# Performance work log

Hardware: AMD Instinct MI355X
Metric: run time of the kernel (lower is better)

Reference implementation:

```python
import jax, jax.numpy as jnp
import numpy as np

N, E, H, L, G, MAX_Z = 100000, 1600000, 128, 3, 1024, 1000
BN_EPS = 1e-5

def setup_inputs() -> dict:
    key = jax.random.key(0)
    ks = jax.random.split(key, 16)
    z = jax.random.randint(ks[0], (N,), 0, MAX_Z)
    edge_index = jax.random.randint(ks[1], (2, E), 0, N)
    batch = jnp.sort(jax.random.randint(ks[2], (N,), 0, G))
    s = 1.0 / np.sqrt(H)
    z_table = jax.random.normal(ks[3], (MAX_Z, H), jnp.float32)
    conv_W1 = jax.random.normal(ks[4], (L, H, H), jnp.float32) * s
    conv_b1 = jnp.zeros((L, H), jnp.float32)
    conv_W2 = jax.random.normal(ks[5], (L, H, H), jnp.float32) * s
    conv_b2 = jnp.zeros((L, H), jnp.float32)
    bn_gamma = jnp.ones((L, H), jnp.float32)
    bn_beta = jnp.zeros((L, H), jnp.float32)
    lin1_W = jax.random.normal(ks[6], (L * H, H), jnp.float32) / np.sqrt(L * H)
    lin1_b = jnp.zeros((H,), jnp.float32)
    lin2_W = jax.random.normal(ks[7], (H, 1), jnp.float32) * s
    lin2_b = jnp.zeros((1,), jnp.float32)
    return {"z": z, "edge_index": edge_index, "batch": batch,
            "z_table": z_table, "conv_W1": conv_W1, "conv_b1": conv_b1,
            "conv_W2": conv_W2, "conv_b2": conv_b2, "bn_gamma": bn_gamma,
            "bn_beta": bn_beta, "lin1_W": lin1_W, "lin1_b": lin1_b,
            "lin2_W": lin2_W, "lin2_b": lin2_b}

def _gin_layer(x, src, dst, W1, b1, W2, b2, gamma, beta):
    # GIN sum aggregation: (1+eps)*x_i + sum_{j->i} x_j  (eps=0)
    agg = x + jax.ops.segment_sum(x[src], dst, num_segments=N)
    h = jax.nn.relu(agg @ W1 + b1)
    h = jax.nn.relu(h @ W2 + b2)
    # BatchNorm1d (training-mode batch statistics over nodes)
    mu = jnp.mean(h, axis=0)
    var = jnp.mean(jnp.square(h - mu), axis=0)
    return gamma * (h - mu) * jax.lax.rsqrt(var + BN_EPS) + beta

def reference(z, edge_index, batch, z_table, conv_W1, conv_b1, conv_W2,
              conv_b2, bn_gamma, bn_beta, lin1_W, lin1_b, lin2_W, lin2_b):
    src, dst = edge_index[0], edge_index[1]
    x = z_table[z]                      # [N, H]
    xs = []
    for l in range(L):
        x = _gin_layer(x, src, dst, conv_W1[l], conv_b1[l], conv_W2[l],
                       conv_b2[l], bn_gamma[l], bn_beta[l])
        xs.append(x)
    feat = jnp.concatenate(xs, axis=1)  # [N, L*H] (jk=True)
    sums = jax.ops.segment_sum(feat, batch, num_segments=G)
    cnt = jax.ops.segment_sum(jnp.ones((N,), feat.dtype), batch, num_segments=G)
    pooled = sums / jnp.maximum(cnt, 1.0)[:, None]   # global_mean_pool [G, L*H]
    h = jax.nn.relu(pooled @ lin1_W + lin1_b)
    # dropout inactive (eval mode)
    return h @ lin2_W + lin2_b          # [G, 1]
```

## Files before the change

kernel.cpp:

```cpp
#include <hip/hip_runtime.h>

#define NN 100000
#define NE 1600000
#define HD 128
#define NL 3
#define NG 1024
#define BN_EPS 1e-5f
#define SCAN_CHUNK 1024

static inline int cdiv(int a, int b) { return (a + b - 1) / b; }

__global__ __launch_bounds__(256) void zero_counts_kernel(int* __restrict__ cnt) {
  int t = blockIdx.x * 256 + threadIdx.x;
  if (t < NN) cnt[t] = 0;
}

__global__ __launch_bounds__(256) void hist_kernel(const int* __restrict__ dstI,
    int* __restrict__ cnt) {
  int e = blockIdx.x * 256 + threadIdx.x;
  if (e < NE) atomicAdd(&cnt[dstI[e]], 1);
}

__global__ __launch_bounds__(256) void scan_block_kernel(const int* __restrict__ cnt,
    int* __restrict__ rowptr, int* __restrict__ bsums) {
  __shared__ int sh[SCAN_CHUNK];
  __shared__ int ts[256];
  int base = blockIdx.x * SCAN_CHUNK;
  for (int i = threadIdx.x; i < SCAN_CHUNK; i += 256)
    sh[i] = (base + i < NN) ? cnt[base + i] : 0;
  __syncthreads();
  int t4 = threadIdx.x * 4;
  int a0 = sh[t4], a1 = sh[t4 + 1], a2 = sh[t4 + 2], a3 = sh[t4 + 3];
  int tsum = a0 + a1 + a2 + a3;
  ts[threadIdx.x] = tsum;
  __syncthreads();
  for (int off = 1; off < 256; off <<= 1) {
    int v = ts[threadIdx.x];
    int u = (threadIdx.x >= off) ? ts[threadIdx.x - off] : 0;
    __syncthreads();
    ts[threadIdx.x] = v + u;
    __syncthreads();
  }
  int texcl = ts[threadIdx.x] - tsum;
  sh[t4] = texcl;
  sh[t4 + 1] = texcl + a0;
  sh[t4 + 2] = texcl + a0 + a1;
  sh[t4 + 3] = texcl + a0 + a1 + a2;
  __syncthreads();
  for (int i = threadIdx.x; i < SCAN_CHUNK; i += 256) {
    int g = base + i;
    if (g < NN) rowptr[g] = sh[i];
  }
  if (threadIdx.x == 255) bsums[blockIdx.x] = ts[255];
}

__global__ void scan_bsums_kernel(int* __restrict__ bsums, int nb) {
  if (threadIdx.x == 0) {
    int run = 0;
    for (int i = 0; i < nb; ++i) { int v = bsums[i]; bsums[i] = run; run += v; }
  }
}

__global__ __launch_bounds__(256) void scan_add_kernel(int* __restrict__ rowptr,
    const int* __restrict__ bsums, int* __restrict__ fill_off) {
  int t = blockIdx.x * 256 + threadIdx.x;
  if (t < NN) {
    int v = rowptr[t] + bsums[t / SCAN_CHUNK];
    rowptr[t] = v;
    fill_off[t] = v;
  }
  if (t == 0) rowptr[NN] = NE;
}

__global__ __launch_bounds__(256) void fill_kernel(const int* __restrict__ srcI,
    const int* __restrict__ dstI, const int* __restrict__ z,
    int* __restrict__ fill_off, int* __restrict__ esrc, int* __restrict__ esrcz) {
  int e = blockIdx.x * 256 + threadIdx.x;
  if (e >= NE) return;
  int s = srcI[e];
  int d = dstI[e];
  int pos = atomicAdd(&fill_off[d], 1);
  esrc[pos] = s;
  esrcz[pos] = z[s];
}

__global__ __launch_bounds__(256) void agg_kernel(const int* __restrict__ rowptr,
    const int* __restrict__ eidx, const float* __restrict__ xsrc, int xstride,
    const int* __restrict__ selfz, float* __restrict__ agg) {
  int n = blockIdx.x * 4 + (threadIdx.x >> 6);
  if (n >= NN) return;
  int lane = threadIdx.x & 63;
  int lo = rowptr[n], hi = rowptr[n + 1];
  int deg = hi - lo;
  int selfrow = selfz ? selfz[n] : n;
  float2 acc = *(const float2*)(xsrc + (size_t)selfrow * xstride + lane * 2);

  for (int base = 0; base < deg; base += 64) {
    int cnt = deg - base; if (cnt > 64) cnt = 64;
    int idx = (base + lane < deg) ? eidx[lo + base + lane] : 0;
    int j = 0;
    for (; j + 4 <= cnt; j += 4) {
      int s0 = __shfl(idx, j, 64);
      int s1 = __shfl(idx, j + 1, 64);
      int s2 = __shfl(idx, j + 2, 64);
      int s3 = __shfl(idx, j + 3, 64);
      float2 v0 = *(const float2*)(xsrc + (size_t)s0 * xstride + lane * 2);
      float2 v1 = *(const float2*)(xsrc + (size_t)s1 * xstride + lane * 2);
      float2 v2 = *(const float2*)(xsrc + (size_t)s2 * xstride + lane * 2);
      float2 v3 = *(const float2*)(xsrc + (size_t)s3 * xstride + lane * 2);
      acc.x += v0.x + v1.x + v2.x + v3.x;
      acc.y += v0.y + v1.y + v2.y + v3.y;
    }
    for (; j < cnt; ++j) {
      int s = __shfl(idx, j, 64);
      float2 v = *(const float2*)(xsrc + (size_t)s * xstride + lane * 2);
      acc.x += v.x; acc.y += v.y;
    }
  }
  *(float2*)(agg + (size_t)n * HD + lane * 2) = acc;
}

template <int STATS>
__global__ __launch_bounds__(256) void gemm_relu_kernel_t(
    const float* __restrict__ A, const float* __restrict__ B,
    const float* __restrict__ bias, float* __restrict__ C, int M,
    double* __restrict__ gsums) {
  __shared__ float As[128][65];
  __shared__ float Bs[32][128];
  __shared__ float csum[256];
  const int tid = threadIdx.x;
  const int row0 = blockIdx.x * 64;

  if (STATS) { csum[tid] = 0.f; }

  #pragma unroll
  for (int i = 0; i < 8; ++i) {
    int f = tid + i * 256;
    int row = f >> 5;
    int kq = (f & 31) << 2;
    int gr = row0 + row;
    float4 v = make_float4(0.f, 0.f, 0.f, 0.f);
    if (gr < M) v = *(const float4*)(A + (size_t)gr * HD + kq);
    As[kq + 0][row] = v.x; As[kq + 1][row] = v.y;
    As[kq + 2][row] = v.z; As[kq + 3][row] = v.w;
  }

  const int colbase = (tid & 15) << 2;
  const int rowbase = (tid >> 4) << 2;
  float acc[4][8] = {};

  for (int kc = 0; kc < 4; ++kc) {
    __syncthreads();
    #pragma unroll
    for (int i = 0; i < 4; ++i) {
      int f = tid + i * 256;
      int k = f >> 5;
      int c4 = (f & 31) << 2;
      *(float4*)(&Bs[k][c4]) = *(const float4*)(B + (size_t)(kc * 32 + k) * HD + c4);
    }
    __syncthreads();
    #pragma unroll
    for (int k = 0; k < 32; ++k) {
      const int kk = kc * 32 + k;
      float a0 = As[kk][rowbase + 0];
      float a1 = As[kk][rowbase + 1];
      float a2 = As[kk][rowbase + 2];
      float a3 = As[kk][rowbase + 3];
      float4 bl = *(const float4*)(&Bs[k][colbase]);
      float4 bh = *(const float4*)(&Bs[k][colbase + 64]);
      acc[0][0] += a0 * bl.x; acc[0][1] += a0 * bl.y; acc[0][2] += a0 * bl.z; acc[0][3] += a0 * bl.w;
      acc[0][4] += a0 * bh.x; acc[0][5] += a0 * bh.y; acc[0][6] += a0 * bh.z; acc[0][7] += a0 * bh.w;
      acc[1][0] += a1 * bl.x; acc[1][1] += a1 * bl.y; acc[1][2] += a1 * bl.z; acc[1][3] += a1 * bl.w;
      acc[1][4] += a1 * bh.x; acc[1][5] += a1 * bh.y; acc[1][6] += a1 * bh.z; acc[1][7] += a1 * bh.w;
      acc[2][0] += a2 * bl.x; acc[2][1] += a2 * bl.y; acc[2][2] += a2 * bl.z; acc[2][3] += a2 * bl.w;
      acc[2][4] += a2 * bh.x; acc[2][5] += a2 * bh.y; acc[2][6] += a2 * bh.z; acc[2][7] += a2 * bh.w;
      acc[3][0] += a3 * bl.x; acc[3][1] += a3 * bl.y; acc[3][2] += a3 * bl.z; acc[3][3] += a3 * bl.w;
      acc[3][4] += a3 * bh.x; acc[3][5] += a3 * bh.y; acc[3][6] += a3 * bh.z; acc[3][7] += a3 * bh.w;
    }
  }

  float4 bvl = *(const float4*)(bias + colbase);
  float4 bvh = *(const float4*)(bias + colbase + 64);
  float ps[8] = {}, pq[8] = {};
  #pragma unroll
  for (int r = 0; r < 4; ++r) {
    int gr = row0 + rowbase + r;
    if (gr < M) {
      float4 o;
      o.x = fmaxf(acc[r][0] + bvl.x, 0.f);
      o.y = fmaxf(acc[r][1] + bvl.y, 0.f);
      o.z = fmaxf(acc[r][2] + bvl.z, 0.f);
      o.w = fmaxf(acc[r][3] + bvl.w, 0.f);
      *(float4*)(C + (size_t)gr * HD + colbase) = o;
      if (STATS) {
        ps[0] += o.x; ps[1] += o.y; ps[2] += o.z; ps[3] += o.w;
        pq[0] += o.x * o.x; pq[1] += o.y * o.y; pq[2] += o.z * o.z; pq[3] += o.w * o.w;
      }
      o.x = fmaxf(acc[r][4] + bvh.x, 0.f);
      o.y = fmaxf(acc[r][5] + bvh.y, 0.f);
      o.z = fmaxf(acc[r][6] + bvh.z, 0.f);
      o.w = fmaxf(acc[r][7] + bvh.w, 0.f);
      *(float4*)(C + (size_t)gr * HD + colbase + 64) = o;
      if (STATS) {
        ps[4] += o.x; ps[5] += o.y; ps[6] += o.z; ps[7] += o.w;
        pq[4] += o.x * o.x; pq[5] += o.y * o.y; pq[6] += o.z * o.z; pq[7] += o.w * o.w;
      }
    }
  }

  if (STATS) {
    __syncthreads();
    #pragma unroll
    for (int c = 0; c < 4; ++c) {
      atomicAdd(&csum[colbase + c], ps[c]);
      atomicAdd(&csum[128 + colbase + c], pq[c]);
      atomicAdd(&csum[colbase + 64 + c], ps[4 + c]);
      atomicAdd(&csum[128 + colbase + 64 + c], pq[4 + c]);
    }
    __syncthreads();
    if (tid < 128) {
      atomicAdd(&gsums[tid], (double)csum[tid]);
      atomicAdd(&gsums[HD + tid], (double)csum[128 + tid]);
    }
  }
}

__global__ void zero_d_kernel(double* p) { p[threadIdx.x] = 0.0; }

__global__ void bn_finalize_kernel(const double* __restrict__ sums,
    const float* __restrict__ gamma, const float* __restrict__ beta,
    float* __restrict__ ss) {
  int c = threadIdx.x;
  double mu = sums[c] * (1.0 / NN);
  double var = sums[HD + c] * (1.0 / NN) - mu * mu;
  float sc = gamma[c] * (float)(1.0 / sqrt(var + (double)BN_EPS));
  ss[c] = sc;
  ss[HD + c] = beta[c] - (float)mu * sc;
}

__global__ __launch_bounds__(256) void bn_apply_kernel(const float* __restrict__ h,
    const float* __restrict__ ss, float* __restrict__ featl) {
  int t = blockIdx.x * 256 + threadIdx.x;
  if (t >= NN * 32) return;
  int row = t >> 5, c4 = (t & 31) << 2;
  float4 v = *(const float4*)(h + (size_t)row * HD + c4);
  float4 sc = *(const float4*)(ss + c4);
  float4 sh = *(const float4*)(ss + HD + c4);
  float4 o;
  o.x = v.x * sc.x + sh.x;
  o.y = v.y * sc.y + sh.y;
  o.z = v.z * sc.z + sh.z;
  o.w = v.w * sc.w + sh.w;
  *(float4*)(featl + (size_t)row * (NL * HD) + c4) = o;
}

__device__ __forceinline__ int lbound(const int* __restrict__ b, int val) {
  int lo = 0, hi = NN;
  while (lo < hi) { int m = (lo + hi) >> 1; if (b[m] < val) lo = m + 1; else hi = m; }
  return lo;
}

__global__ __launch_bounds__(384) void pool_kernel(const int* __restrict__ batch,
    const float* __restrict__ feat, float* __restrict__ pooled) {
  int g = blockIdx.x;
  int lo = lbound(batch, g), hi = lbound(batch, g + 1);
  float s = 0.f;
  for (int r = lo; r < hi; ++r) s += feat[(size_t)r * (NL * HD) + threadIdx.x];
  float inv = 1.f / (float)max(hi - lo, 1);
  pooled[(size_t)g * (NL * HD) + threadIdx.x] = s * inv;
}

__global__ __launch_bounds__(128) void mlp_kernel(const float* __restrict__ pooled,
    const float* __restrict__ W1, const float* __restrict__ b1,
    const float* __restrict__ W2, const float* __restrict__ b2,
    float* __restrict__ out) {
  int g = blockIdx.x, c = threadIdx.x;
  const float* p = pooled + (size_t)g * (NL * HD);
  float acc = b1[c];
  #pragma unroll 4
  for (int k = 0; k < NL * HD; ++k) acc = fmaf(p[k], W1[(size_t)k * HD + c], acc);
  acc = fmaxf(acc, 0.f);
  float prod = acc * W2[c];
  #pragma unroll
  for (int off = 32; off > 0; off >>= 1) prod += __shfl_xor(prod, off, 64);
  __shared__ float part[2];
  if ((c & 63) == 0) part[c >> 6] = prod;
  __syncthreads();
  if (c == 0) out[g] = part[0] + part[1] + b2[0];
}

extern "C" void kernel_launch(void* const* d_in, const int* in_sizes, int n_in,
                              void* d_out, int out_size, void* d_ws, size_t ws_size,
                              hipStream_t stream) {
  (void)in_sizes; (void)n_in; (void)out_size; (void)ws_size;
  const int*   z     = (const int*)d_in[0];
  const int*   ei    = (const int*)d_in[1];
  const int*   batch = (const int*)d_in[2];
  const float* ztab  = (const float*)d_in[3];
  const float* W1    = (const float*)d_in[4];
  const float* b1    = (const float*)d_in[5];
  const float* W2    = (const float*)d_in[6];
  const float* b2    = (const float*)d_in[7];
  const float* gamma = (const float*)d_in[8];
  const float* beta  = (const float*)d_in[9];
  const float* l1W   = (const float*)d_in[10];
  const float* l1b   = (const float*)d_in[11];
  const float* l2W   = (const float*)d_in[12];
  const float* l2b   = (const float*)d_in[13];
  float* out = (float*)d_out;

  char* w = (char*)d_ws;
  float*  bufA   = (float*)w;  w += (size_t)NN * HD * 4;
  float*  bufB   = (float*)w;  w += (size_t)NN * HD * 4;
  float*  feat   = (float*)w;  w += (size_t)NN * (NL * HD) * 4;
  float*  pooled = (float*)w;  w += (size_t)NG * (NL * HD) * 4;
  double* sums   = (double*)w; w += 256 * 8;
  float*  sshift = (float*)w;  w += 256 * 4;
  int*    rowptr = (int*)w;    w += (size_t)(NN + 1) * 4;
  int*    counts = (int*)w;    w += (size_t)NN * 4;
  int*    filloff= (int*)w;    w += (size_t)NN * 4;
  int*    esrc   = (int*)w;    w += (size_t)NE * 4;
  int*    bsums  = (int*)w;    w += (size_t)cdiv(NN, SCAN_CHUNK) * 4;
  int* esrcz = (int*)bufA;

  const int* srcI = ei;
  const int* dstI = ei + NE;

  dim3 blk(256);
  const int g_nh = cdiv(NN * 32, 256);
  const int g_nn = cdiv(NN, 256);
  const int g_ne = cdiv(NE, 256);
  const int nb_scan = cdiv(NN, SCAN_CHUNK);

  zero_counts_kernel<<<g_nn, blk, 0, stream>>>(counts);
  hist_kernel<<<g_ne, blk, 0, stream>>>(dstI, counts);
  scan_block_kernel<<<nb_scan, blk, 0, stream>>>(counts, rowptr, bsums);
  scan_bsums_kernel<<<1, 64, 0, stream>>>(bsums, nb_scan);
  scan_add_kernel<<<g_nn, blk, 0, stream>>>(rowptr, bsums, filloff);
  fill_kernel<<<g_ne, blk, 0, stream>>>(srcI, dstI, z, filloff, esrc, esrcz);

  for (int l = 0; l < NL; ++l) {
    float* aggbuf = (l & 1) ? bufA : bufB;
    float* tmpbuf = (l & 1) ? bufB : bufA;

    if (l == 0) {
      agg_kernel<<<cdiv(NN, 4), blk, 0, stream>>>(rowptr, esrcz, ztab, HD, z, aggbuf);
    } else {
      agg_kernel<<<cdiv(NN, 4), blk, 0, stream>>>(rowptr, esrc,
          feat + (l - 1) * HD, NL * HD, nullptr, aggbuf);
    }
    gemm_relu_kernel_t<0><<<cdiv(NN, 64), blk, 0, stream>>>(aggbuf,
        W1 + (size_t)l * HD * HD, b1 + l * HD, tmpbuf, NN, nullptr);
    zero_d_kernel<<<1, 256, 0, stream>>>(sums);
    gemm_relu_kernel_t<1><<<cdiv(NN, 64), blk, 0, stream>>>(tmpbuf,
        W2 + (size_t)l * HD * HD, b2 + l * HD, aggbuf, NN, sums);
    bn_finalize_kernel<<<1, 128, 0, stream>>>(sums, gamma + l * HD, beta + l * HD, sshift);
    bn_apply_kernel<<<g_nh, blk, 0, stream>>>(aggbuf, sshift, feat + l * HD);
  }

  pool_kernel<<<NG, 384, 0, stream>>>(batch, feat, pooled);
  mlp_kernel<<<NG, 128, 0, stream>>>(pooled, l1W, l1b, l2W, l2b, out);
}
```

Before: 1.200 ms.

## Fold BatchNorm affine into aggregation and pooling; use 128x128 GEMM tiles

Drops the standalone BN-apply pass. The second GEMM now writes the raw ReLU output straight into the concatenated feature buffer. The per-channel scale and shift are applied later, at aggregation time as scale*sum + (deg+1)*shift, and in the pooling kernel, which is exact because the affine is linear. The GEMM is also retiled to 128 rows per block, with an 8x8 register tile per thread and A loaded per k-chunk, to raise arithmetic intensity. This removes one full read and write of the hidden activations per layer, at the cost of more registers per thread and possibly lower occupancy.

```diff
diff --git a/kernel.cpp b/kernel.cpp
--- a/kernel.cpp
+++ b/kernel.cpp
@@ -86,7 +86,8 @@
 
 __global__ __launch_bounds__(256) void agg_kernel(const int* __restrict__ rowptr,
     const int* __restrict__ eidx, const float* __restrict__ xsrc, int xstride,
-    const int* __restrict__ selfz, float* __restrict__ agg) {
+    const int* __restrict__ selfz, const float* __restrict__ ss,
+    float* __restrict__ agg) {
   int n = blockIdx.x * 4 + (threadIdx.x >> 6);
   if (n >= NN) return;
   int lane = threadIdx.x & 63;
@@ -117,105 +118,96 @@
       acc.x += v.x; acc.y += v.y;
     }
   }
-  *(float2*)(agg + (size_t)n * HD + lane * 2) = acc;
+
+  float2 o = acc;
+  if (ss) {
+    float scx = ss[lane * 2], scy = ss[lane * 2 + 1];
+    float shx = ss[128 + lane * 2], shy = ss[129 + lane * 2];
+    float cntf = (float)(deg + 1);
+    o.x = acc.x * scx + cntf * shx;
+    o.y = acc.y * scy + cntf * shy;
+  }
+  *(float2*)(agg + (size_t)n * HD + lane * 2) = o;
 }
 
 template <int STATS>
-__global__ __launch_bounds__(256) void gemm_relu_kernel_t(
+__global__ __launch_bounds__(256) void gemm128_kernel(
     const float* __restrict__ A, const float* __restrict__ B,
-    const float* __restrict__ bias, float* __restrict__ C, int M,
+    const float* __restrict__ bias, float* __restrict__ C, int cstride, int M,
     double* __restrict__ gsums) {
-  __shared__ float As[128][65];
-  __shared__ float Bs[32][128];
+  __shared__ float As[32][136];
+  __shared__ float Bs[32][136];
   __shared__ float csum[256];
   const int tid = threadIdx.x;
-  const int row0 = blockIdx.x * 64;
-
-  if (STATS) { csum[tid] = 0.f; }
-
-  #pragma unroll
-  for (int i = 0; i < 8; ++i) {
-    int f = tid + i * 256;
-    int row = f >> 5;
-    int kq = (f & 31) << 2;
-    int gr = row0 + row;
-    float4 v = make_float4(0.f, 0.f, 0.f, 0.f);
-    if (gr < M) v = *(const float4*)(A + (size_t)gr * HD + kq);
-    As[kq + 0][row] = v.x; As[kq + 1][row] = v.y;
-    As[kq + 2][row] = v.z; As[kq + 3][row] = v.w;
-  }
-
-  const int colbase = (tid & 15) << 2;
-  const int rowbase = (tid >> 4) << 2;
-  float acc[4][8] = {};
+  const int row0 = blockIdx.x * 128;
+  const int tr = tid >> 4;
+  const int tc = tid & 15;
+
+  if (STATS) csum[tid] = 0.f;
+
+  float acc[8][8] = {};
 
   for (int kc = 0; kc < 4; ++kc) {
     __syncthreads();
     #pragma unroll
     for (int i = 0; i < 4; ++i) {
       int f = tid + i * 256;
-      int k = f >> 5;
-      int c4 = (f & 31) << 2;
+      int row = f >> 3, kq = f & 7;
+      int gr = row0 + row;
+      float4 v = make_float4(0.f, 0.f, 0.f, 0.f);
+      if (gr < M) v = *(const float4*)(A + (size_t)gr * HD + kc * 32 + kq * 4);
+      As[kq * 4 + 0][row] = v.x; As[kq * 4 + 1][row] = v.y;
+      As[kq * 4 + 2][row] = v.z; As[kq * 4 + 3][row] = v.w;
+    }
+    #pragma unroll
+    for (int i = 0; i < 4; ++i) {
+      int f = tid + i * 256;
+      int k = f >> 5, c4 = (f & 31) << 2;
       *(float4*)(&Bs[k][c4]) = *(const float4*)(B + (size_t)(kc * 32 + k) * HD + c4);
     }
     __syncthreads();
     #pragma unroll
     for (int k = 0; k < 32; ++k) {
-      const int kk = kc * 32 + k;
-      float a0 = As[kk][rowbase + 0];
-      float a1 = As[kk][rowbase + 1];
-      float a2 = As[kk][rowbase + 2];
-      float a3 = As[kk][rowbase + 3];
-      float4 bl = *(const float4*)(&Bs[k][colbase]);
-      float4 bh = *(const float4*)(&Bs[k][colbase + 64]);
-      acc[0][0] += a0 * bl.x; acc[0][1] += a0 * bl.y; acc[0][2] += a0 * bl.z; acc[0][3] += a0 * bl.w;
-      acc[0][4] += a0 * bh.x; acc[0][5] += a0 * bh.y; acc[0][6] += a0 * bh.z; acc[0][7] += a0 * bh.w;
-      acc[1][0] += a1 * bl.x; acc[1][1] += a1 * bl.y; acc[1][2] += a1 * bl.z; acc[1][3] += a1 * bl.w;
-      acc[1][4] += a1 * bh.x; acc[1][5] += a1 * bh.y; acc[1][6] += a1 * bh.z; acc[1][7] += a1 * bh.w;
-      acc[2][0] += a2 * bl.x; acc[2][1] += a2 * bl.y; acc[2][2] += a2 * bl.z; acc[2][3] += a2 * bl.w;
-      acc[2][4] += a2 * bh.x; acc[2][5] += a2 * bh.y; acc[2][6] += a2 * bh.z; acc[2][7] += a2 * bh.w;
-      acc[3][0] += a3 * bl.x; acc[3][1] += a3 * bl.y; acc[3][2] += a3 * bl.z; acc[3][3] += a3 * bl.w;
-      acc[3][4] += a3 * bh.x; acc[3][5] += a3 * bh.y; acc[3][6] += a3 * bh.z; acc[3][7] += a3 * bh.w;
-    }
-  }
-
-  float4 bvl = *(const float4*)(bias + colbase);
-  float4 bvh = *(const float4*)(bias + colbase + 64);
+      float4 a0 = *(const float4*)(&As[k][tr * 8]);
+      float4 a1 = *(const float4*)(&As[k][tr * 8 + 4]);
+      float4 b0 = *(const float4*)(&Bs[k][tc * 8]);
+      float4 b1 = *(const float4*)(&Bs[k][tc * 8 + 4]);
+      float av[8] = {a0.x, a0.y, a0.z, a0.w, a1.x, a1.y, a1.z, a1.w};
+      float bv[8] = {b0.x, b0.y, b0.z, b0.w, b1.x, b1.y, b1.z, b1.w};
+      #pragma unroll
+      for (int r = 0; r < 8; ++r)
+        #pragma unroll
+        for (int c = 0; c < 8; ++c)
+          acc[r][c] += av[r] * bv[c];
+    }
+  }
+
+  float4 bv0 = *(const float4*)(bias + tc * 8);
+  float4 bv1 = *(const float4*)(bias + tc * 8 + 4);
+  float bb[8] = {bv0.x, bv0.y, bv0.z, bv0.w, bv1.x, bv1.y, bv1.z, bv1.w};
   float ps[8] = {}, pq[8] = {};
   #pragma unroll
-  for (int r = 0; r < 4; ++r) {
-    int gr = row0 + rowbase + r;
+  for (int r = 0; r < 8; ++r) {
+    int gr = row0 + tr * 8 + r;
     if (gr < M) {
-      float4 o;
-      o.x = fmaxf(acc[r][0] + bvl.x, 0.f);
-      o.y = fmaxf(acc[r][1] + bvl.y, 0.f);
-      o.z = fmaxf(acc[r][2] + bvl.z, 0.f);
-      o.w = fmaxf(acc[r][3] + bvl.w, 0.f);
-      *(float4*)(C + (size_t)gr * HD + colbase) = o;
+      float o[8];
+      #pragma unroll
+      for (int c = 0; c < 8; ++c) o[c] = fmaxf(acc[r][c] + bb[c], 0.f);
+      *(float4*)(C + (size_t)gr * cstride + tc * 8)     = make_float4(o[0], o[1], o[2], o[3]);
+      *(float4*)(C + (size_t)gr * cstride + tc * 8 + 4) = make_float4(o[4], o[5], o[6], o[7]);
       if (STATS) {
-        ps[0] += o.x; ps[1] += o.y; ps[2] += o.z; ps[3] += o.w;
-        pq[0] += o.x * o.x; pq[1] += o.y * o.y; pq[2] += o.z * o.z; pq[3] += o.w * o.w;
+        #pragma unroll
+        for (int c = 0; c < 8; ++c) { ps[c] += o[c]; pq[c] += o[c] * o[c]; }
       }
-      o.x = fmaxf(acc[r][4] + bvh.x, 0.f);
-      o.y = fmaxf(acc[r][5] + bvh.y, 0.f);
-      o.z = fmaxf(acc[r][6] + bvh.z, 0.f);
-      o.w = fmaxf(acc[r][7] + bvh.w, 0.f);
-      *(float4*)(C + (size_t)gr * HD + colbase + 64) = o;
-      if (STATS) {
-        ps[4] += o.x; ps[5] += o.y; ps[6] += o.z; ps[7] += o.w;
-        pq[4] += o.x * o.x; pq[5] += o.y * o.y; pq[6] += o.z * o.z; pq[7] += o.w * o.w;
-      }
     }
   }
 
   if (STATS) {
     __syncthreads();
     #pragma unroll
-    for (int c = 0; c < 4; ++c) {
-      atomicAdd(&csum[colbase + c], ps[c]);
-      atomicAdd(&csum[128 + colbase + c], pq[c]);
-      atomicAdd(&csum[colbase + 64 + c], ps[4 + c]);
-      atomicAdd(&csum[128 + colbase + 64 + c], pq[4 + c]);
+    for (int c = 0; c < 8; ++c) {
+      atomicAdd(&csum[tc * 8 + c], ps[c]);
+      atomicAdd(&csum[128 + tc * 8 + c], pq[c]);
     }
     __syncthreads();
     if (tid < 128) {
@@ -238,22 +230,6 @@
   ss[HD + c] = beta[c] - (float)mu * sc;
 }
 
-__global__ __launch_bounds__(256) void bn_apply_kernel(const float* __restrict__ h,
-    const float* __restrict__ ss, float* __restrict__ featl) {
-  int t = blockIdx.x * 256 + threadIdx.x;
-  if (t >= NN * 32) return;
-  int row = t >> 5, c4 = (t & 31) << 2;
-  float4 v = *(const float4*)(h + (size_t)row * HD + c4);
-  float4 sc = *(const float4*)(ss + c4);
-  float4 sh = *(const float4*)(ss + HD + c4);
-  float4 o;
-  o.x = v.x * sc.x + sh.x;
-  o.y = v.y * sc.y + sh.y;
-  o.z = v.z * sc.z + sh.z;
-  o.w = v.w * sc.w + sh.w;
-  *(float4*)(featl + (size_t)row * (NL * HD) + c4) = o;
-}
-
 __device__ __forceinline__ int lbound(const int* __restrict__ b, int val) {
   int lo = 0, hi = NN;
   while (lo < hi) { int m = (lo + hi) >> 1; if (b[m] < val) lo = m + 1; else hi = m; }
@@ -261,13 +237,17 @@
 }
 
 __global__ __launch_bounds__(384) void pool_kernel(const int* __restrict__ batch,
-    const float* __restrict__ feat, float* __restrict__ pooled) {
+    const float* __restrict__ feat, const float* __restrict__ ssAll,
+    float* __restrict__ pooled) {
   int g = blockIdx.x;
+  int c = threadIdx.x;
+  int l = c >> 7, cc = c & 127;
+  float sc = ssAll[l * 256 + cc], sh = ssAll[l * 256 + 128 + cc];
   int lo = lbound(batch, g), hi = lbound(batch, g + 1);
   float s = 0.f;
-  for (int r = lo; r < hi; ++r) s += feat[(size_t)r * (NL * HD) + threadIdx.x];
+  for (int r = lo; r < hi; ++r) s += feat[(size_t)r * (NL * HD) + c];
   float inv = 1.f / (float)max(hi - lo, 1);
-  pooled[(size_t)g * (NL * HD) + threadIdx.x] = s * inv;
+  pooled[(size_t)g * (NL * HD) + c] = sc * (s * inv) + sh;
 }
 
 __global__ __launch_bounds__(128) void mlp_kernel(const float* __restrict__ pooled,
@@ -315,7 +295,7 @@
   float*  feat   = (float*)w;  w += (size_t)NN * (NL * HD) * 4;
   float*  pooled = (float*)w;  w += (size_t)NG * (NL * HD) * 4;
   double* sums   = (double*)w; w += 256 * 8;
-  float*  sshift = (float*)w;  w += 256 * 4;
+  float*  ssAll  = (float*)w;  w += (size_t)NL * 256 * 4;
   int*    rowptr = (int*)w;    w += (size_t)(NN + 1) * 4;
   int*    counts = (int*)w;    w += (size_t)NN * 4;
   int*    filloff= (int*)w;    w += (size_t)NN * 4;
@@ -327,10 +307,10 @@
   const int* dstI = ei + NE;
 
   dim3 blk(256);
-  const int g_nh = cdiv(NN * 32, 256);
   const int g_nn = cdiv(NN, 256);
   const int g_ne = cdiv(NE, 256);
   const int nb_scan = cdiv(NN, SCAN_CHUNK);
+  const int g_gemm = cdiv(NN, 128);
 
   zero_counts_kernel<<<g_nn, blk, 0, stream>>>(counts);
   hist_kernel<<<g_ne, blk, 0, stream>>>(dstI, counts);
@@ -340,24 +320,22 @@
   fill_kernel<<<g_ne, blk, 0, stream>>>(srcI, dstI, z, filloff, esrc, esrcz);
 
   for (int l = 0; l < NL; ++l) {
-    float* aggbuf = (l & 1) ? bufA : bufB;
-    float* tmpbuf = (l & 1) ? bufB : bufA;
-
     if (l == 0) {
-      agg_kernel<<<cdiv(NN, 4), blk, 0, stream>>>(rowptr, esrcz, ztab, HD, z, aggbuf);
+      agg_kernel<<<cdiv(NN, 4), blk, 0, stream>>>(rowptr, esrcz, ztab, HD,
+                                                  z, nullptr, bufB);
     } else {
       agg_kernel<<<cdiv(NN, 4), blk, 0, stream>>>(rowptr, esrc,
-          feat + (l - 1) * HD, NL * HD, nullptr, aggbuf);
-    }
-    gemm_relu_kernel_t<0><<<cdiv(NN, 64), blk, 0, stream>>>(aggbuf,
-        W1 + (size_t)l * HD * HD, b1 + l * HD, tmpbuf, NN, nullptr);
+          feat + (l - 1) * HD, NL * HD, nullptr, ssAll + (l - 1) * 256, bufB);
+    }
+    gemm128_kernel<0><<<g_gemm, blk, 0, stream>>>(bufB,
+        W1 + (size_t)l * HD * HD, b1 + l * HD, bufA, HD, NN, nullptr);
     zero_d_kernel<<<1, 256, 0, stream>>>(sums);
-    gemm_relu_kernel_t<1><<<cdiv(NN, 64), blk, 0, stream>>>(tmpbuf,
-        W2 + (size_t)l * HD * HD, b2 + l * HD, aggbuf, NN, sums);
-    bn_finalize_kernel<<<1, 128, 0, stream>>>(sums, gamma + l * HD, beta + l * HD, sshift);
-    bn_apply_kernel<<<g_nh, blk, 0, stream>>>(aggbuf, sshift, feat + l * HD);
-  }
-
-  pool_kernel<<<NG, 384, 0, stream>>>(batch, feat, pooled);
+    gemm128_kernel<1><<<g_gemm, blk, 0, stream>>>(bufA,
+        W2 + (size_t)l * HD * HD, b2 + l * HD, feat + l * HD, NL * HD, NN, sums);
+    bn_finalize_kernel<<<1, 128, 0, stream>>>(sums, gamma + l * HD,
+                                              beta + l * HD, ssAll + l * 256);
+  }
+
+  pool_kernel<<<NG, 384, 0, stream>>>(batch, feat, ssAll, pooled);
   mlp_kernel<<<NG, 128, 0, stream>>>(pooled, l1W, l1b, l2W, l2b, out);
 }
```

After: 1.141 ms. -4.9%, faster.
